# Optimization experiments

Hardware: AMD Instinct MI355X
Metric: run time of the kernel (lower is better)

Reference implementation:

```python
import jax, jax.numpy as jnp
import numpy as np

NUM_PARTS = 10
COS_W = 10.0
COS_K = 100.0
EPS = 1e-6

B, V, F, VHD = 512, 6890, 13776, 20000


def setup_inputs() -> dict:
    key = jax.random.key(0)
    k1, k2, k3, k4, k5 = jax.random.split(key, 5)
    vertices = jax.random.normal(k1, (B, V, 3), dtype=jnp.float32)
    bary = jax.random.uniform(k2, (VHD, 3), dtype=jnp.float32)
    faces = jax.random.randint(k3, (F, 3), 0, V)
    hd_fid = jax.random.randint(k4, (VHD,), 0, F)
    part_fid = jax.random.randint(k5, (F,), 0, NUM_PARTS)
    return {"vertices": vertices, "bary": bary, "faces": faces,
            "hd_fid": hd_fid, "part_fid": part_fid}


def reference(vertices, bary, faces, hd_fid, part_fid):
    # --- per-part mesh volume (signed tetra volumes, segment-summed by part) ---
    tri = vertices[:, faces]                       # [B, F, 3, 3] gather face corners
    t0, t1, t2 = tri[:, :, 0], tri[:, :, 1], tri[:, :, 2]
    vol_f = jnp.einsum('bfi,bfi->bf', jnp.cross(t0, t1), t2) / 6.0   # [B, F]
    fid_onehot = jax.nn.one_hot(part_fid, NUM_PARTS, dtype=vertices.dtype)  # [F, P]
    per_part_volume = vol_f @ fid_onehot           # [B, P]

    # --- HDfy: barycentric sampling of HD vertices on faces ---
    w = bary / jnp.sum(bary, axis=-1, keepdims=True)          # barycentric weights [VHD,3]
    vidx = faces[hd_fid]                                       # [VHD, 3]
    hd_corners = vertices[:, vidx]                             # [B, VHD, 3, 3]
    vertices_hd = jnp.einsum('bvkd,vk->bvd', hd_corners, w)    # [B, VHD, 3]

    # --- per-HD-vertex part volume (bmm with one-hot == gather) ---
    hd_part = part_fid[hd_fid]                                 # [VHD]
    vol_hd = per_part_volume[:, hd_part]                       # [B, VHD]

    # --- center of mass ---
    com = jnp.sum(vertices_hd * vol_hd[..., None], axis=1) / jnp.sum(vol_hd, axis=1, keepdims=True)  # [B,3]

    # --- center of pressure via height-based pressure weights ---
    h = vertices_hd[:, :, 1]                                   # [B, VHD], ground plane at y=0
    inside = (h < 0.0).astype(vertices_hd.dtype)
    outside = (h >= 0.0).astype(vertices_hd.dtype)
    pw = inside * (1.0 - COS_K * h) + outside * jnp.exp(-COS_W * h)
    cop = jnp.sum(vertices_hd * pw[..., None], axis=1) / (jnp.sum(pw, axis=1, keepdims=True) + EPS)  # [B,3]

    # --- stability loss: xz distance between COM and COP ---
    d = com - cop
    return jnp.sqrt(d[:, 0] ** 2 + d[:, 2] ** 2)               # [B]
```

## Files before the change

### kernel.cpp

```cpp
#include <hip/hip_runtime.h>
#include <math.h>

#define NB     512
#define NV     6890
#define NF     13776
#define NVHD   20000
#define NPARTS 10
#define NTHREADS 1024
#define NWAVES (NTHREADS/64)
#define CUT    6698

__global__ void build_tables(const float* __restrict__ bary,
                             const int*   __restrict__ faces,
                             const int*   __restrict__ hd_fid,
                             const int*   __restrict__ part_fid,
                             uint2* __restrict__ f_pack,
                             uint4* __restrict__ hd_pack)
{
    int i = blockIdx.x * blockDim.x + threadIdx.x;
    if (i < NF) {
        unsigned a = (unsigned)faces[3*i+0] | ((unsigned)faces[3*i+1] << 16);
        unsigned b = (unsigned)faces[3*i+2] | ((unsigned)part_fid[i]  << 16);
        f_pack[i] = make_uint2(a, b);
    }
    if (i < NVHD) {
        int fid = hd_fid[i];
        unsigned a = (unsigned)faces[3*fid+0] | ((unsigned)faces[3*fid+1] << 16);
        unsigned b = (unsigned)faces[3*fid+2] | ((unsigned)part_fid[fid]  << 16);
        float b0 = bary[3*i+0], b1 = bary[3*i+1], b2 = bary[3*i+2];
        float inv = 1.0f / (b0 + b1 + b2);
        hd_pack[i] = make_uint4(a, b, __float_as_uint(b0*inv), __float_as_uint(b1*inv));
    }
}

__global__ __launch_bounds__(NTHREADS, 8) void stab_kernel(
    const float* __restrict__ vertices,
    const uint2* __restrict__ f_pack,
    const uint4* __restrict__ hd_pack,
    float*       __restrict__ out)
{
    __shared__ float2 sxy[CUT];
    __shared__ float  szz[CUT];
    __shared__ float  spart[NPARTS];
    __shared__ float  sredp[NWAVES][NPARTS];

    const int tid  = threadIdx.x;
    const int b    = blockIdx.x;
    const int wave = tid >> 6;
    const int lane = tid & 63;
    const float* __restrict__ vb = vertices + (size_t)b * (NV * 3);

    for (int v = tid; v < CUT; v += NTHREADS) {
        float x = vb[3 * v + 0];
        float y = vb[3 * v + 1];
        float z = vb[3 * v + 2];
        sxy[v] = make_float2(x, y);
        szz[v] = z;
    }
    __syncthreads();

#define GETV(idx, X, Y, Z) do {                                   \
        int _ic = (idx) < CUT ? (idx) : CUT - 1;                  \
        float2 _t = sxy[_ic]; float _z = szz[_ic];                \
        X = _t.x; Y = _t.y; Z = _z;                               \
        if ((idx) >= CUT) {                                       \
            X = vb[3*(idx)+0]; Y = vb[3*(idx)+1]; Z = vb[3*(idx)+2]; \
        }                                                         \
    } while (0)

    float accp[NPARTS];
    #pragma unroll
    for (int q = 0; q < NPARTS; q++) accp[q] = 0.f;

    #pragma unroll 2
    for (int f = tid; f < NF; f += NTHREADS) {
        uint2 ft = f_pack[f];
        int i0 = ft.x & 0xFFFF, i1 = ft.x >> 16;
        int i2 = ft.y & 0xFFFF, p  = ft.y >> 16;
        float x0, y0, z0, x1, y1, z1, x2, y2, z2;
        GETV(i0, x0, y0, z0);
        GETV(i1, x1, y1, z1);
        GETV(i2, x2, y2, z2);
        float cx = y0 * z1 - z0 * y1;
        float cy = z0 * x1 - x0 * z1;
        float cz = x0 * y1 - y0 * x1;
        float vol = (cx * x2 + cy * y2 + cz * z2) * (1.0f / 6.0f);
        #pragma unroll
        for (int q = 0; q < NPARTS; q++) accp[q] += (p == q) ? vol : 0.f;
    }
    #pragma unroll
    for (int q = 0; q < NPARTS; q++) {
        float s = accp[q];
        #pragma unroll
        for (int off = 32; off > 0; off >>= 1) s += __shfl_down(s, off, 64);
        accp[q] = s;
    }
    if (lane == 0) {
        #pragma unroll
        for (int q = 0; q < NPARTS; q++) sredp[wave][q] = accp[q];
    }
    __syncthreads();
    if (tid < NPARTS) {
        float s = 0.f;
        #pragma unroll
        for (int w = 0; w < NWAVES; w++) s += sredp[w][tid];
        spart[tid] = s;
    }
    __syncthreads();

    float sVx = 0.f, sVy = 0.f, sVz = 0.f, sVol = 0.f;
    float sPx = 0.f, sPy = 0.f, sPz = 0.f, sPw  = 0.f;

    #pragma unroll 2
    for (int v = tid; v < NVHD; v += NTHREADS) {
        uint4 hp = hd_pack[v];
        int i0 = hp.x & 0xFFFF, i1 = hp.x >> 16;
        int i2 = hp.y & 0xFFFF, p  = hp.y >> 16;
        float w0 = __uint_as_float(hp.z);
        float w1 = __uint_as_float(hp.w);
        float w2 = 1.0f - w0 - w1;
        float x0, y0, z0, x1, y1, z1, x2, y2, z2;
        GETV(i0, x0, y0, z0);
        GETV(i1, x1, y1, z1);
        GETV(i2, x2, y2, z2);
        float x = w0 * x0 + w1 * x1 + w2 * x2;
        float y = w0 * y0 + w1 * y1 + w2 * y2;
        float z = w0 * z0 + w1 * z1 + w2 * z2;
        float vol = spart[p];
        float pw  = (y < 0.f) ? fmaf(-100.f, y, 1.f) : __expf(-10.f * y);
        sVx += x * vol;  sVy += y * vol;  sVz += z * vol;  sVol += vol;
        sPx += x * pw;   sPy += y * pw;   sPz += z * pw;   sPw  += pw;
    }

    float vals[8] = {sVx, sVy, sVz, sVol, sPx, sPy, sPz, sPw};
    #pragma unroll
    for (int q = 0; q < 8; q++) {
        float s = vals[q];
        #pragma unroll
        for (int off = 32; off > 0; off >>= 1) s += __shfl_down(s, off, 64);
        vals[q] = s;
    }
    float* sred8 = &sredp[0][0];
    if (lane == 0) {
        #pragma unroll
        for (int q = 0; q < 8; q++) sred8[wave * 8 + q] = vals[q];
    }
    __syncthreads();
    if (tid == 0) {
        float r[8];
        #pragma unroll
        for (int q = 0; q < 8; q++) {
            float s = 0.f;
            #pragma unroll
            for (int w = 0; w < NWAVES; w++) s += sred8[w * 8 + q];
            r[q] = s;
        }
        float invVol = 1.0f / r[3];
        float invPw  = 1.0f / (r[7] + 1e-6f);
        float comx = r[0] * invVol, comz = r[2] * invVol;
        float copx = r[4] * invPw,  copz = r[6] * invPw;
        float d0 = comx - copx, d2 = comz - copz;
        out[b] = sqrtf(d0 * d0 + d2 * d2);
    }
#undef GETV
}

extern "C" void kernel_launch(void* const* d_in, const int* in_sizes, int n_in,
                              void* d_out, int out_size, void* d_ws, size_t ws_size,
                              hipStream_t stream) {
    const float* vertices = (const float*)d_in[0];
    const float* bary     = (const float*)d_in[1];
    const int*   faces    = (const int*)d_in[2];
    const int*   hd_fid   = (const int*)d_in[3];
    const int*   part_fid = (const int*)d_in[4];
    float* out = (float*)d_out;

    char* ws = (char*)d_ws;
    uint2* f_pack  = (uint2*)ws;
    uint4* hd_pack = (uint4*)(ws + (size_t)NF * 8);

    build_tables<<<(NVHD + 255) / 256, 256, 0, stream>>>(bary, faces, hd_fid, part_fid,
                                                         f_pack, hd_pack);
    stab_kernel<<<NB, NTHREADS, 0, stream>>>(vertices, f_pack, hd_pack, out);
}
```

Before: 59.03 us.

## Radix-sort HD vertex table by face id and raise loop unrolling

Adds a three-pass, single-block 5-bit LSD radix sort that reorders the HD vertex pack table by face id before the main kernel runs. Sorted entries make neighbouring threads read nearby vertices from shared and global memory, which is meant to improve locality and cut LDS bank conflicts. The face and HD loops are also unrolled by 4 instead of 2. The cost is three extra serial single-block launches per call and higher register pressure in the main kernel.

```diff
diff --git a/kernel.cpp b/kernel.cpp
--- a/kernel.cpp
+++ b/kernel.cpp
@@ -9,13 +9,15 @@
 #define NTHREADS 1024
 #define NWAVES (NTHREADS/64)
 #define CUT    6698
+#define NCH    ((NVHD + 63) / 64)
 
 __global__ void build_tables(const float* __restrict__ bary,
                              const int*   __restrict__ faces,
                              const int*   __restrict__ hd_fid,
                              const int*   __restrict__ part_fid,
                              uint2* __restrict__ f_pack,
-                             uint4* __restrict__ hd_pack)
+                             uint4* __restrict__ hd_pack,
+                             unsigned* __restrict__ hd_key)
 {
     int i = blockIdx.x * blockDim.x + threadIdx.x;
     if (i < NF) {
@@ -30,6 +32,85 @@
         float b0 = bary[3*i+0], b1 = bary[3*i+1], b2 = bary[3*i+2];
         float inv = 1.0f / (b0 + b1 + b2);
         hd_pack[i] = make_uint4(a, b, __float_as_uint(b0*inv), __float_as_uint(b1*inv));
+        hd_key[i]  = (unsigned)fid;
+    }
+}
+
+__global__ __launch_bounds__(1024) void radix_pass(
+    const uint4*    __restrict__ in_pack,
+    const unsigned* __restrict__ in_key,
+    uint4*          __restrict__ out_pack,
+    unsigned*       __restrict__ out_key,
+    int shift)
+{
+    __shared__ unsigned hist[32][NCH];
+    __shared__ unsigned tot[32];
+    __shared__ unsigned base[32];
+    const int tid = threadIdx.x, wave = tid >> 6, lane = tid & 63;
+    const unsigned long long lowmask = (1ull << lane) - 1ull;
+
+    for (int k = tid; k < 32 * NCH; k += 1024) (&hist[0][0])[k] = 0u;
+    __syncthreads();
+
+    for (int c = wave; c < NCH; c += NWAVES) {
+        int i = c * 64 + lane;
+        bool valid = i < NVHD;
+        unsigned d = valid ? ((in_key[i] >> shift) & 31u) : 0u;
+        unsigned long long m = ~0ull;
+        #pragma unroll
+        for (int b = 0; b < 5; b++) {
+            unsigned long long bb = __ballot(valid && ((d >> b) & 1u));
+            m &= ((d >> b) & 1u) ? bb : ~bb;
+        }
+        m &= __ballot(valid);
+        if (valid && (m & lowmask) == 0ull)
+            hist[d][c] = (unsigned)__popcll(m);
+    }
+    __syncthreads();
+
+    for (int r = wave; r < 32; r += NWAVES) {
+        unsigned carry = 0;
+        #pragma unroll
+        for (int seg = 0; seg < (NCH + 63) / 64; seg++) {
+            int idx = seg * 64 + lane;
+            unsigned v = (idx < NCH) ? hist[r][idx] : 0u;
+            unsigned incl = v;
+            #pragma unroll
+            for (int off = 1; off < 64; off <<= 1) {
+                unsigned n = __shfl_up(incl, off, 64);
+                if (lane >= off) incl += n;
+            }
+            if (idx < NCH) hist[r][idx] = incl - v + carry;
+            carry += __shfl(incl, 63, 64);
+        }
+        if (lane == 0) tot[r] = carry;
+    }
+    __syncthreads();
+    if (tid == 0) {
+        unsigned r = 0;
+        #pragma unroll
+        for (int d = 0; d < 32; d++) { base[d] = r; r += tot[d]; }
+    }
+    __syncthreads();
+
+    for (int c = wave; c < NCH; c += NWAVES) {
+        int i = c * 64 + lane;
+        bool valid = i < NVHD;
+        unsigned key = valid ? in_key[i] : 0u;
+        unsigned d = (key >> shift) & 31u;
+        unsigned long long m = ~0ull;
+        #pragma unroll
+        for (int b = 0; b < 5; b++) {
+            unsigned long long bb = __ballot(valid && ((d >> b) & 1u));
+            m &= ((d >> b) & 1u) ? bb : ~bb;
+        }
+        m &= __ballot(valid);
+        if (valid) {
+            unsigned rank = (unsigned)__popcll(m & lowmask);
+            unsigned pos = base[d] + hist[d][c] + rank;
+            out_key[pos]  = key;
+            out_pack[pos] = in_pack[i];
+        }
     }
 }
 
@@ -72,7 +153,7 @@
     #pragma unroll
     for (int q = 0; q < NPARTS; q++) accp[q] = 0.f;
 
-    #pragma unroll 2
+    #pragma unroll 4
     for (int f = tid; f < NF; f += NTHREADS) {
         uint2 ft = f_pack[f];
         int i0 = ft.x & 0xFFFF, i1 = ft.x >> 16;
@@ -111,7 +192,7 @@
     float sVx = 0.f, sVy = 0.f, sVz = 0.f, sVol = 0.f;
     float sPx = 0.f, sPy = 0.f, sPz = 0.f, sPw  = 0.f;
 
-    #pragma unroll 2
+    #pragma unroll 4
     for (int v = tid; v < NVHD; v += NTHREADS) {
         uint4 hp = hd_pack[v];
         int i0 = hp.x & 0xFFFF, i1 = hp.x >> 16;
@@ -176,10 +257,17 @@
     float* out = (float*)d_out;
 
     char* ws = (char*)d_ws;
-    uint2* f_pack  = (uint2*)ws;
-    uint4* hd_pack = (uint4*)(ws + (size_t)NF * 8);
+    uint2*    f_pack = (uint2*)ws;                       size_t off = (size_t)NF * 8;
+    uint4*    packA  = (uint4*)(ws + off);               off += (size_t)NVHD * 16;
+    uint4*    packB  = (uint4*)(ws + off);               off += (size_t)NVHD * 16;
+    unsigned* keyA   = (unsigned*)(ws + off);            off += (size_t)NVHD * 4;
+    unsigned* keyB   = (unsigned*)(ws + off);            off += (size_t)NVHD * 4;
 
     build_tables<<<(NVHD + 255) / 256, 256, 0, stream>>>(bary, faces, hd_fid, part_fid,
-                                                         f_pack, hd_pack);
-    stab_kernel<<<NB, NTHREADS, 0, stream>>>(vertices, f_pack, hd_pack, out);
-}
+                                                         f_pack, packA, keyA);
+    radix_pass<<<1, 1024, 0, stream>>>(packA, keyA, packB, keyB, 0);
+    radix_pass<<<1, 1024, 0, stream>>>(packB, keyB, packA, keyA, 5);
+    radix_pass<<<1, 1024, 0, stream>>>(packA, keyA, packB, keyB, 10);
+
+    stab_kernel<<<NB, NTHREADS, 0, stream>>>(vertices, f_pack, packB, out);
+}
```

New measurement: 165.8 us. +180.9%, slower.

## Cache most-referenced vertices in LDS via usage-count based vertex renumbering

Applied to the files above, without the earlier changes.

Counts how often each vertex is referenced by faces and HD samples, then computes a permutation so the least-used vertices are the ones evicted from the LDS cache. Index tables are rewritten into the new numbering, and the main kernel stages vertices by permuted slot. Global-memory fallback reads for uncached vertices should become rarer. This adds several small preprocessing launches, including a single-wave selection kernel, plus an extra newid lookup during staging. Unroll factors also go from 2 to 4.

```diff
diff --git a/kernel.cpp b/kernel.cpp
--- a/kernel.cpp
+++ b/kernel.cpp
@@ -8,28 +8,106 @@
 #define NPARTS 10
 #define NTHREADS 1024
 #define NWAVES (NTHREADS/64)
-#define CUT    6698
+#define CAP    6768
+#define NEVICT (NV - CAP)
+
+__global__ void zero_cnt(int* __restrict__ cnt) {
+    int i = blockIdx.x * blockDim.x + threadIdx.x;
+    if (i < NV) cnt[i] = 0;
+}
 
 __global__ void build_tables(const float* __restrict__ bary,
                              const int*   __restrict__ faces,
                              const int*   __restrict__ hd_fid,
                              const int*   __restrict__ part_fid,
                              uint2* __restrict__ f_pack,
-                             uint4* __restrict__ hd_pack)
+                             uint4* __restrict__ hd_pack,
+                             int*   __restrict__ cnt)
 {
     int i = blockIdx.x * blockDim.x + threadIdx.x;
     if (i < NF) {
-        unsigned a = (unsigned)faces[3*i+0] | ((unsigned)faces[3*i+1] << 16);
-        unsigned b = (unsigned)faces[3*i+2] | ((unsigned)part_fid[i]  << 16);
-        f_pack[i] = make_uint2(a, b);
+        int i0 = faces[3*i+0], i1 = faces[3*i+1], i2 = faces[3*i+2];
+        f_pack[i] = make_uint2((unsigned)i0 | ((unsigned)i1 << 16),
+                               (unsigned)i2 | ((unsigned)part_fid[i] << 16));
+        atomicAdd(&cnt[i0], 1); atomicAdd(&cnt[i1], 1); atomicAdd(&cnt[i2], 1);
     }
     if (i < NVHD) {
         int fid = hd_fid[i];
-        unsigned a = (unsigned)faces[3*fid+0] | ((unsigned)faces[3*fid+1] << 16);
-        unsigned b = (unsigned)faces[3*fid+2] | ((unsigned)part_fid[fid]  << 16);
+        int i0 = faces[3*fid+0], i1 = faces[3*fid+1], i2 = faces[3*fid+2];
         float b0 = bary[3*i+0], b1 = bary[3*i+1], b2 = bary[3*i+2];
         float inv = 1.0f / (b0 + b1 + b2);
-        hd_pack[i] = make_uint4(a, b, __float_as_uint(b0*inv), __float_as_uint(b1*inv));
+        hd_pack[i] = make_uint4((unsigned)i0 | ((unsigned)i1 << 16),
+                                (unsigned)i2 | ((unsigned)part_fid[fid] << 16),
+                                __float_as_uint(b0*inv), __float_as_uint(b1*inv));
+        atomicAdd(&cnt[i0], 1); atomicAdd(&cnt[i1], 1); atomicAdd(&cnt[i2], 1);
+    }
+}
+
+__global__ __launch_bounds__(64) void select_perm(
+    const int* __restrict__ cnt,
+    int* __restrict__ newid,
+    int* __restrict__ old_of_new)
+{
+    __shared__ int hist[64 * 64];
+    __shared__ int tr[2];
+    const int lane = threadIdx.x;
+    const int per  = (NV + 63) / 64;
+    const int beg  = lane * per;
+    const int end  = (beg + per < NV) ? beg + per : NV;
+
+    for (int b = 0; b < 64; b++) hist[lane * 64 + b] = 0;
+    __syncthreads();
+    for (int v = beg; v < end; v++) {
+        int c = cnt[v]; c = c > 63 ? 63 : c;
+        hist[lane * 64 + c]++;
+    }
+    __syncthreads();
+    int tot = 0;
+    for (int l = 0; l < 64; l++) tot += hist[l * 64 + lane];
+    int incl = tot;
+    for (int off = 1; off < 64; off <<= 1) { int n = __shfl_up(incl, off, 64); if (lane >= off) incl += n; }
+    int under = incl - tot;
+    if (under <= NEVICT && NEVICT < under + tot) { tr[0] = lane; tr[1] = NEVICT - under; }
+    __syncthreads();
+    const int t = tr[0], r = tr[1];
+
+    int a = 0, e = 0;
+    for (int v = beg; v < end; v++) {
+        int c = cnt[v]; c = c > 63 ? 63 : c;
+        a += (c > t); e += (c == t);
+    }
+    int A = a; for (int off = 1; off < 64; off <<= 1) { int n = __shfl_up(A, off, 64); if (lane >= off) A += n; } A -= a;
+    int E = e; for (int off = 1; off < 64; off <<= 1) { int n = __shfl_up(E, off, 64); if (lane >= off) E += n; } E -= e;
+
+    int a_run = A, e_run = E;
+    for (int v = beg; v < end; v++) {
+        int c = cnt[v]; c = c > 63 ? 63 : c;
+        int eq_kept_before = e_run - r > 0 ? e_run - r : 0;
+        int kb = a_run + eq_kept_before;
+        bool kept = (c > t) || (c == t && e_run >= r);
+        int slot = kept ? kb : (CAP + (v - kb));
+        newid[v] = slot;
+        old_of_new[slot] = v;
+        if (c > t) a_run++; else if (c == t) e_run++;
+    }
+}
+
+__global__ void rewrite_tables(uint2* __restrict__ f_pack,
+                               uint4* __restrict__ hd_pack,
+                               const int* __restrict__ newid)
+{
+    int i = blockIdx.x * blockDim.x + threadIdx.x;
+    if (i < NF) {
+        uint2 ft = f_pack[i];
+        unsigned i0 = newid[ft.x & 0xFFFF], i1 = newid[ft.x >> 16];
+        unsigned i2 = newid[ft.y & 0xFFFF], p  = ft.y >> 16;
+        f_pack[i] = make_uint2(i0 | (i1 << 16), i2 | (p << 16));
+    }
+    if (i < NVHD) {
+        uint4 hp = hd_pack[i];
+        unsigned i0 = newid[hp.x & 0xFFFF], i1 = newid[hp.x >> 16];
+        unsigned i2 = newid[hp.y & 0xFFFF], p  = hp.y >> 16;
+        hd_pack[i] = make_uint4(i0 | (i1 << 16), i2 | (p << 16), hp.z, hp.w);
     }
 }
 
@@ -37,10 +115,12 @@
     const float* __restrict__ vertices,
     const uint2* __restrict__ f_pack,
     const uint4* __restrict__ hd_pack,
+    const int*   __restrict__ newid,
+    const int*   __restrict__ old_of_new,
     float*       __restrict__ out)
 {
-    __shared__ float2 sxy[CUT];
-    __shared__ float  szz[CUT];
+    __shared__ float2 sxy[CAP];
+    __shared__ float  szz[CAP];
     __shared__ float  spart[NPARTS];
     __shared__ float  sredp[NWAVES][NPARTS];
 
@@ -50,29 +130,30 @@
     const int lane = tid & 63;
     const float* __restrict__ vb = vertices + (size_t)b * (NV * 3);
 
-    for (int v = tid; v < CUT; v += NTHREADS) {
+    for (int v = tid; v < NV; v += NTHREADS) {
         float x = vb[3 * v + 0];
         float y = vb[3 * v + 1];
         float z = vb[3 * v + 2];
-        sxy[v] = make_float2(x, y);
-        szz[v] = z;
-    }
-    __syncthreads();
-
-#define GETV(idx, X, Y, Z) do {                                   \
-        int _ic = (idx) < CUT ? (idx) : CUT - 1;                  \
-        float2 _t = sxy[_ic]; float _z = szz[_ic];                \
-        X = _t.x; Y = _t.y; Z = _z;                               \
-        if ((idx) >= CUT) {                                       \
-            X = vb[3*(idx)+0]; Y = vb[3*(idx)+1]; Z = vb[3*(idx)+2]; \
-        }                                                         \
+        int s = newid[v];
+        if (s < CAP) { sxy[s] = make_float2(x, y); szz[s] = z; }
+    }
+    __syncthreads();
+
+#define GETV(idx, X, Y, Z) do {                                     \
+        int _s = (idx); int _c = _s < CAP ? _s : 0;                 \
+        float2 _t = sxy[_c]; float _z = szz[_c];                    \
+        X = _t.x; Y = _t.y; Z = _z;                                 \
+        if (_s >= CAP) {                                            \
+            int _o = old_of_new[_s];                                \
+            X = vb[3*_o+0]; Y = vb[3*_o+1]; Z = vb[3*_o+2];         \
+        }                                                           \
     } while (0)
 
     float accp[NPARTS];
     #pragma unroll
     for (int q = 0; q < NPARTS; q++) accp[q] = 0.f;
 
-    #pragma unroll 2
+    #pragma unroll 4
     for (int f = tid; f < NF; f += NTHREADS) {
         uint2 ft = f_pack[f];
         int i0 = ft.x & 0xFFFF, i1 = ft.x >> 16;
@@ -111,7 +192,7 @@
     float sVx = 0.f, sVy = 0.f, sVz = 0.f, sVol = 0.f;
     float sPx = 0.f, sPy = 0.f, sPz = 0.f, sPw  = 0.f;
 
-    #pragma unroll 2
+    #pragma unroll 4
     for (int v = tid; v < NVHD; v += NTHREADS) {
         uint4 hp = hd_pack[v];
         int i0 = hp.x & 0xFFFF, i1 = hp.x >> 16;
@@ -176,10 +257,17 @@
     float* out = (float*)d_out;
 
     char* ws = (char*)d_ws;
-    uint2* f_pack  = (uint2*)ws;
-    uint4* hd_pack = (uint4*)(ws + (size_t)NF * 8);
-
+    uint2* f_pack      = (uint2*)ws;              size_t off = (size_t)NF * 8;
+    uint4* hd_pack     = (uint4*)(ws + off);      off += (size_t)NVHD * 16;
+    int*   cnt         = (int*)(ws + off);        off += (size_t)NV * 4;
+    int*   newid       = (int*)(ws + off);        off += (size_t)NV * 4;
+    int*   old_of_new  = (int*)(ws + off);        off += (size_t)NV * 4;
+
+    zero_cnt<<<(NV + 1023) / 1024, 1024, 0, stream>>>(cnt);
     build_tables<<<(NVHD + 255) / 256, 256, 0, stream>>>(bary, faces, hd_fid, part_fid,
-                                                         f_pack, hd_pack);
-    stab_kernel<<<NB, NTHREADS, 0, stream>>>(vertices, f_pack, hd_pack, out);
-}
+                                                         f_pack, hd_pack, cnt);
+    select_perm<<<1, 64, 0, stream>>>(cnt, newid, old_of_new);
+    rewrite_tables<<<(NVHD + 255) / 256, 256, 0, stream>>>(f_pack, hd_pack, newid);
+
+    stab_kernel<<<NB, NTHREADS, 0, stream>>>(vertices, f_pack, hd_pack, newid, old_of_new, out);
+}
```

Result: slower. 145.4 us (+146.3%).

## Sort faces by part so face volume accumulation is wave-uniform

Applied to the files above, without the earlier changes.

Adds a single-block kernel that stable-partitions the face table by part id, using ballot-based per-chunk counts and prefix sums. The main kernel then checks whether all lanes in a wave share the same part and, if so, adds the volume into one accumulator instead of running a 10-way select. It also drops the unused y-moment accumulators and raises the HD loop unroll to 4. The trade-off is an extra serial single-block launch before the main kernel and a longer divergent code path in the main loop.

```diff
diff --git a/kernel.cpp b/kernel.cpp
--- a/kernel.cpp
+++ b/kernel.cpp
@@ -9,27 +9,97 @@
 #define NTHREADS 1024
 #define NWAVES (NTHREADS/64)
 #define CUT    6698
+#define NCHF   ((NF + 63) / 64)
+
+__global__ __launch_bounds__(1024) void sort_faces(
+    const int* __restrict__ faces,
+    const int* __restrict__ part_fid,
+    uint2*     __restrict__ f_sorted)
+{
+    __shared__ unsigned chunkoff[NPARTS][NCHF];
+    __shared__ unsigned pbase[NPARTS];
+    const int tid = threadIdx.x, wave = tid >> 6, lane = tid & 63;
+    const unsigned long long lowmask = (1ull << lane) - 1ull;
+
+    for (int k = tid; k < NPARTS * NCHF; k += 1024) (&chunkoff[0][0])[k] = 0u;
+    __syncthreads();
+
+    for (int c = wave; c < NCHF; c += NWAVES) {
+        int i = c * 64 + lane;
+        bool valid = i < NF;
+        unsigned p = valid ? (unsigned)part_fid[i] : 0u;
+        unsigned long long m = ~0ull;
+        #pragma unroll
+        for (int b = 0; b < 4; b++) {
+            unsigned long long bb = __ballot(valid && ((p >> b) & 1u));
+            m &= ((p >> b) & 1u) ? bb : ~bb;
+        }
+        m &= __ballot(valid);
+        if (valid && (m & lowmask) == 0ull)
+            chunkoff[p][c] = (unsigned)__popcll(m);
+    }
+    __syncthreads();
+
+    if (wave < NPARTS) {
+        unsigned carry = 0;
+        #pragma unroll
+        for (int seg = 0; seg < (NCHF + 63) / 64; seg++) {
+            int idx = seg * 64 + lane;
+            unsigned v = (idx < NCHF) ? chunkoff[wave][idx] : 0u;
+            unsigned incl = v;
+            #pragma unroll
+            for (int off = 1; off < 64; off <<= 1) {
+                unsigned n = __shfl_up(incl, off, 64);
+                if (lane >= off) incl += n;
+            }
+            if (idx < NCHF) chunkoff[wave][idx] = incl - v + carry;
+            carry += __shfl(incl, 63, 64);
+        }
+        if (lane == 0) pbase[wave] = carry;
+    }
+    __syncthreads();
+    if (tid == 0) {
+        unsigned r = 0;
+        #pragma unroll
+        for (int p = 0; p < NPARTS; p++) { unsigned t = pbase[p]; pbase[p] = r; r += t; }
+    }
+    __syncthreads();
+
+    for (int c = wave; c < NCHF; c += NWAVES) {
+        int i = c * 64 + lane;
+        bool valid = i < NF;
+        unsigned p = valid ? (unsigned)part_fid[i] : 0u;
+        unsigned long long m = ~0ull;
+        #pragma unroll
+        for (int b = 0; b < 4; b++) {
+            unsigned long long bb = __ballot(valid && ((p >> b) & 1u));
+            m &= ((p >> b) & 1u) ? bb : ~bb;
+        }
+        m &= __ballot(valid);
+        if (valid) {
+            unsigned rank = (unsigned)__popcll(m & lowmask);
+            unsigned pos = pbase[p] + chunkoff[p][c] + rank;
+            f_sorted[pos] = make_uint2(
+                (unsigned)faces[3*i+0] | ((unsigned)faces[3*i+1] << 16),
+                (unsigned)faces[3*i+2] | (p << 16));
+        }
+    }
+}
 
 __global__ void build_tables(const float* __restrict__ bary,
                              const int*   __restrict__ faces,
                              const int*   __restrict__ hd_fid,
                              const int*   __restrict__ part_fid,
-                             uint2* __restrict__ f_pack,
                              uint4* __restrict__ hd_pack)
 {
     int i = blockIdx.x * blockDim.x + threadIdx.x;
-    if (i < NF) {
-        unsigned a = (unsigned)faces[3*i+0] | ((unsigned)faces[3*i+1] << 16);
-        unsigned b = (unsigned)faces[3*i+2] | ((unsigned)part_fid[i]  << 16);
-        f_pack[i] = make_uint2(a, b);
-    }
     if (i < NVHD) {
         int fid = hd_fid[i];
-        unsigned a = (unsigned)faces[3*fid+0] | ((unsigned)faces[3*fid+1] << 16);
-        unsigned b = (unsigned)faces[3*fid+2] | ((unsigned)part_fid[fid]  << 16);
         float b0 = bary[3*i+0], b1 = bary[3*i+1], b2 = bary[3*i+2];
         float inv = 1.0f / (b0 + b1 + b2);
-        hd_pack[i] = make_uint4(a, b, __float_as_uint(b0*inv), __float_as_uint(b1*inv));
+        hd_pack[i] = make_uint4((unsigned)faces[3*fid+0] | ((unsigned)faces[3*fid+1] << 16),
+                                (unsigned)faces[3*fid+2] | ((unsigned)part_fid[fid] << 16),
+                                __float_as_uint(b0*inv), __float_as_uint(b1*inv));
     }
 }
 
@@ -59,13 +129,13 @@
     }
     __syncthreads();
 
-#define GETV(idx, X, Y, Z) do {                                   \
-        int _ic = (idx) < CUT ? (idx) : CUT - 1;                  \
-        float2 _t = sxy[_ic]; float _z = szz[_ic];                \
-        X = _t.x; Y = _t.y; Z = _z;                               \
-        if ((idx) >= CUT) {                                       \
-            X = vb[3*(idx)+0]; Y = vb[3*(idx)+1]; Z = vb[3*(idx)+2]; \
-        }                                                         \
+#define GETV(idx, X, Y, Z) do {                                     \
+        int _s = (idx); int _c = _s < CUT ? _s : CUT - 1;           \
+        float2 _t = sxy[_c]; float _z = szz[_c];                    \
+        X = _t.x; Y = _t.y; Z = _z;                                 \
+        if (_s >= CUT) {                                            \
+            X = vb[3*_s+0]; Y = vb[3*_s+1]; Z = vb[3*_s+2];         \
+        }                                                           \
     } while (0)
 
     float accp[NPARTS];
@@ -76,7 +146,7 @@
     for (int f = tid; f < NF; f += NTHREADS) {
         uint2 ft = f_pack[f];
         int i0 = ft.x & 0xFFFF, i1 = ft.x >> 16;
-        int i2 = ft.y & 0xFFFF, p  = ft.y >> 16;
+        int i2 = ft.y & 0xFFFF, p  = (int)(ft.y >> 16);
         float x0, y0, z0, x1, y1, z1, x2, y2, z2;
         GETV(i0, x0, y0, z0);
         GETV(i1, x1, y1, z1);
@@ -85,8 +155,24 @@
         float cy = z0 * x1 - x0 * z1;
         float cz = x0 * y1 - y0 * x1;
         float vol = (cx * x2 + cy * y2 + cz * z2) * (1.0f / 6.0f);
-        #pragma unroll
-        for (int q = 0; q < NPARTS; q++) accp[q] += (p == q) ? vol : 0.f;
+        int pu = __builtin_amdgcn_readfirstlane(p);
+        if (__all(p == pu)) {
+            switch (pu) {
+                case 0: accp[0] += vol; break;
+                case 1: accp[1] += vol; break;
+                case 2: accp[2] += vol; break;
+                case 3: accp[3] += vol; break;
+                case 4: accp[4] += vol; break;
+                case 5: accp[5] += vol; break;
+                case 6: accp[6] += vol; break;
+                case 7: accp[7] += vol; break;
+                case 8: accp[8] += vol; break;
+                default: accp[9] += vol; break;
+            }
+        } else {
+            #pragma unroll
+            for (int q = 0; q < NPARTS; q++) accp[q] += (p == q) ? vol : 0.f;
+        }
     }
     #pragma unroll
     for (int q = 0; q < NPARTS; q++) {
@@ -108,10 +194,10 @@
     }
     __syncthreads();
 
-    float sVx = 0.f, sVy = 0.f, sVz = 0.f, sVol = 0.f;
-    float sPx = 0.f, sPy = 0.f, sPz = 0.f, sPw  = 0.f;
-
-    #pragma unroll 2
+    float sVx = 0.f, sVz = 0.f, sVol = 0.f;
+    float sPx = 0.f, sPz = 0.f, sPw  = 0.f;
+
+    #pragma unroll 4
     for (int v = tid; v < NVHD; v += NTHREADS) {
         uint4 hp = hd_pack[v];
         int i0 = hp.x & 0xFFFF, i1 = hp.x >> 16;
@@ -128,37 +214,37 @@
         float z = w0 * z0 + w1 * z1 + w2 * z2;
         float vol = spart[p];
         float pw  = (y < 0.f) ? fmaf(-100.f, y, 1.f) : __expf(-10.f * y);
-        sVx += x * vol;  sVy += y * vol;  sVz += z * vol;  sVol += vol;
-        sPx += x * pw;   sPy += y * pw;   sPz += z * pw;   sPw  += pw;
-    }
-
-    float vals[8] = {sVx, sVy, sVz, sVol, sPx, sPy, sPz, sPw};
+        sVx += x * vol;  sVz += z * vol;  sVol += vol;
+        sPx += x * pw;   sPz += z * pw;   sPw  += pw;
+    }
+
+    float vals[6] = {sVx, sVz, sVol, sPx, sPz, sPw};
     #pragma unroll
-    for (int q = 0; q < 8; q++) {
+    for (int q = 0; q < 6; q++) {
         float s = vals[q];
         #pragma unroll
         for (int off = 32; off > 0; off >>= 1) s += __shfl_down(s, off, 64);
         vals[q] = s;
     }
-    float* sred8 = &sredp[0][0];
+    float* sred6 = &sredp[0][0];
     if (lane == 0) {
         #pragma unroll
-        for (int q = 0; q < 8; q++) sred8[wave * 8 + q] = vals[q];
+        for (int q = 0; q < 6; q++) sred6[wave * 6 + q] = vals[q];
     }
     __syncthreads();
     if (tid == 0) {
-        float r[8];
-        #pragma unroll
-        for (int q = 0; q < 8; q++) {
+        float r[6];
+        #pragma unroll
+        for (int q = 0; q < 6; q++) {
             float s = 0.f;
             #pragma unroll
-            for (int w = 0; w < NWAVES; w++) s += sred8[w * 8 + q];
+            for (int w = 0; w < NWAVES; w++) s += sred6[w * 6 + q];
             r[q] = s;
         }
-        float invVol = 1.0f / r[3];
-        float invPw  = 1.0f / (r[7] + 1e-6f);
-        float comx = r[0] * invVol, comz = r[2] * invVol;
-        float copx = r[4] * invPw,  copz = r[6] * invPw;
+        float invVol = 1.0f / r[2];
+        float invPw  = 1.0f / (r[5] + 1e-6f);
+        float comx = r[0] * invVol, comz = r[1] * invVol;
+        float copx = r[3] * invPw,  copz = r[4] * invPw;
         float d0 = comx - copx, d2 = comz - copz;
         out[b] = sqrtf(d0 * d0 + d2 * d2);
     }
@@ -179,7 +265,7 @@
     uint2* f_pack  = (uint2*)ws;
     uint4* hd_pack = (uint4*)(ws + (size_t)NF * 8);
 
-    build_tables<<<(NVHD + 255) / 256, 256, 0, stream>>>(bary, faces, hd_fid, part_fid,
-                                                         f_pack, hd_pack);
+    sort_faces<<<1, 1024, 0, stream>>>(faces, part_fid, f_pack);
+    build_tables<<<(NVHD + 255) / 256, 256, 0, stream>>>(bary, faces, hd_fid, part_fid, hd_pack);
     stab_kernel<<<NB, NTHREADS, 0, stream>>>(vertices, f_pack, hd_pack, out);
 }
```

Result: slower. 78.23 us (+32.5%).
